# Kernel optimization log

Hardware: AMD Instinct MI355X
Metric: run time of the kernel (lower is better)

The kernel has to match this reference:

```python
import jax, jax.numpy as jnp
import numpy as np

EPS = 1e-5
AVG_D_LOG = 2.302585092994046  # avg_d['log'] = log(10)

N, D, F, FE = 65536, 16, 64, 16
POST_IN = (4 * 3 + 1) * F  # (n_agg*n_scalers + 1) * in_dim = 832


def setup_inputs() -> dict:
    key = jax.random.key(0)
    ks = jax.random.split(key, 8)
    h = jax.random.normal(ks[0], (N, F), dtype=jnp.float32)
    edge_attr = jax.random.normal(ks[1], (N, D, FE), dtype=jnp.float32)
    nbr_idx = jax.random.randint(ks[2], (N, D), 0, N)
    pre_in = 2 * F + FE
    W_pre = jax.random.normal(ks[3], (pre_in, F), dtype=jnp.float32) / np.sqrt(pre_in)
    b_pre = jnp.zeros((F,), dtype=jnp.float32)
    W_post1 = jax.random.normal(ks[4], (POST_IN, F), dtype=jnp.float32) / np.sqrt(POST_IN)
    b_post1 = jnp.zeros((F,), dtype=jnp.float32)
    W_post2 = jax.random.normal(ks[5], (F, F), dtype=jnp.float32) / np.sqrt(F)
    b_post2 = jnp.zeros((F,), dtype=jnp.float32)
    return {"h": h, "edge_attr": edge_attr, "nbr_idx": nbr_idx,
            "W_pre": W_pre, "b_pre": b_pre,
            "W_post1": W_post1, "b_post1": b_post1,
            "W_post2": W_post2, "b_post2": b_post2}


def reference(h, edge_attr, nbr_idx, W_pre, b_pre, W_post1, b_post1, W_post2, b_post2):
    # pretrans: message MLP on cat([src_feat, dst_feat, edge_attr])
    h_src = h[nbr_idx]                                   # [N, D, F]
    h_dst = jnp.broadcast_to(h[:, None, :], h_src.shape)  # [N, D, F]
    z = jnp.concatenate([h_src, h_dst, edge_attr], axis=-1)  # [N, D, 2F+FE]
    e = jax.nn.relu(jnp.einsum('ndi,io->ndo', z, W_pre) + b_pre)  # [N, D, F]

    # multi-aggregator neighbor reduction (dim=-2)
    mean = jnp.mean(e, axis=-2)
    mx = jnp.max(e, axis=-2)
    mn = jnp.min(e, axis=-2)
    var = jax.nn.relu(jnp.mean(e * e, axis=-2) - mean * mean)
    std = jnp.sqrt(var + EPS)
    agg = jnp.concatenate([mean, mx, mn, std], axis=-1)  # [N, 4F]

    # degree scalers (fixed in-degree D)
    logD = jnp.asarray(np.log(D + 1.0), dtype=h.dtype)
    amp = agg * (logD / AVG_D_LOG)
    att = agg * (AVG_D_LOG / logD)
    agg = jnp.concatenate([agg, amp, att], axis=-1)      # [N, 12F]

    # posttrans MLP on cat([h, aggregated]) with residual (in_dim == out_dim)
    x = jnp.concatenate([h, agg], axis=-1)               # [N, 13F]
    x = jax.nn.relu(x @ W_post1 + b_post1)
    x = x @ W_post2 + b_post2
    return x + h
```

## Files before the change

kernel.cpp:

```cpp
#include <hip/hip_runtime.h>
#include <hip/hip_bf16.h>
#include <math.h>
#include <stdint.h>


#define N_NODES 65536
#define NBLK (N_NODES / 16)
#define NITER 4
#define GRID_MAIN (NBLK / NITER)
#define GRID_PREP (NBLK + 64)
#define ASTRIDE 348
#define YSTRIDE 76

typedef float f32x4 __attribute__((ext_vector_type(4)));
typedef float f32x16 __attribute__((ext_vector_type(16)));
typedef short s16x8 __attribute__((ext_vector_type(8)));
typedef unsigned short us4 __attribute__((ext_vector_type(4)));

#define GLL16(SRC, DST)                                                        \
    __builtin_amdgcn_global_load_lds(                                          \
        (const __attribute__((address_space(1))) void*)(SRC),                  \
        (__attribute__((address_space(3))) void*)(DST), 16, 0, 0)

__device__ __forceinline__ unsigned short f2bf(float f) {
    union { float f; unsigned int u; } v; v.f = f;
    unsigned int r = v.u + 0x7fffu + ((v.u >> 16) & 1u);
    return (unsigned short)(r >> 16);
}
__device__ __forceinline__ unsigned short f2bfh(float f) {
    __hip_bfloat16 b = __float2bfloat16(f);
    union { __hip_bfloat16 b; unsigned short u; } v; v.b = b; return v.u;
}
__device__ __forceinline__ float bf2f(unsigned short u) {
    union { unsigned int u; float f; } v; v.u = ((unsigned int)u) << 16; return v.f;
}
__device__ __forceinline__ unsigned char enc_u8(float x) {
    int q = __float2int_rn(x * 16.f) + 128;
    q = q < 0 ? 0 : (q > 255 ? 255 : q);
    return (unsigned char)q;
}

__global__ __launch_bounds__(256) void k_prep(const float* __restrict__ h,
                                              const float* __restrict__ Wpre,
                                              const float* __restrict__ b_pre,
                                              const float* __restrict__ Wp1,
                                              const float* __restrict__ Wp2,
                                              unsigned char* __restrict__ u8,
                                              unsigned short* __restrict__ vbf,
                                              unsigned short* __restrict__ wfullT,
                                              unsigned short* __restrict__ w3T,
                                              unsigned short* __restrict__ wp2T,
                                              float c1, float c2) {
    int t = threadIdx.x;
    if (blockIdx.x >= NBLK) {
        int c = blockIdx.x - NBLK;
        for (int k = t; k < 320; k += 256) {
            float v;
            if (k < 64) v = Wp1[k * 64 + c];
            else {
                int kk = k - 64;
                v = Wp1[(64 + kk) * 64 + c] + c1 * Wp1[(320 + kk) * 64 + c]
                                            + c2 * Wp1[(576 + kk) * 64 + c];
            }
            wfullT[c * 320 + k] = f2bf(v);
        }
        if (t < 16)              w3T[c * 16 + t]         = f2bf(Wpre[(128 + t) * 64 + c]);
        if (t >= 64 && t < 128)  wp2T[c * 64 + (t - 64)] = f2bf(Wp2[(t - 64) * 64 + c]);
        return;
    }

    __shared__ unsigned short hl[16 * 68];
    int lane = t & 63;
    int wv = __builtin_amdgcn_readfirstlane(t) >> 6;
    int c = lane & 15, g = lane >> 4;
    int node0 = blockIdx.x * 16;
    {
        int r = t >> 4, q = t & 15;
        float4 hv = *((const float4*)(h + (size_t)node0 * 64) + t);
        us4 o;
        o.x = f2bfh(hv.x); o.y = f2bfh(hv.y); o.z = f2bfh(hv.z); o.w = f2bfh(hv.w);
        *(us4*)&hl[r * 68 + q * 4] = o;
    }
    s16x8 bf[2][2];
    int woff = (wv < 2) ? 0 : 64;
    #pragma unroll
    for (int i2 = 0; i2 < 2; ++i2) {
        int wcol = ((wv & 1) * 32) + i2 * 16 + c;
        #pragma unroll
        for (int ks = 0; ks < 2; ++ks) {
            #pragma unroll
            for (int j = 0; j < 8; ++j)
                bf[i2][ks][j] = (short)f2bfh(Wpre[(woff + ks * 32 + g * 8 + j) * 64 + wcol]);
        }
    }
    __syncthreads();
    f32x4 acc0 = {0.f, 0.f, 0.f, 0.f}, acc1 = {0.f, 0.f, 0.f, 0.f};
    #pragma unroll
    for (int ks = 0; ks < 2; ++ks) {
        s16x8 a = *(const s16x8*)&hl[c * 68 + ks * 32 + g * 8];
        acc0 = __builtin_amdgcn_mfma_f32_16x16x32_bf16(a, bf[0][ks], acc0, 0, 0, 0);
        acc1 = __builtin_amdgcn_mfma_f32_16x16x32_bf16(a, bf[1][ks], acc1, 0, 0, 0);
    }
    #pragma unroll
    for (int i2 = 0; i2 < 2; ++i2) {
        int dcol = ((wv & 1) * 32) + i2 * 16 + c;
        const f32x4& av = i2 ? acc1 : acc0;
        if (wv < 2) {
            float bp = b_pre[dcol];
            #pragma unroll
            for (int i = 0; i < 4; ++i) {
                int row = g * 4 + i;
                u8[(size_t)(node0 + row) * 64 + dcol] = enc_u8(av[i] + bp);
            }
        } else {
            #pragma unroll
            for (int i = 0; i < 4; ++i) {
                int row = g * 4 + i;
                vbf[(size_t)(node0 + row) * 64 + dcol] = f2bfh(av[i]);
            }
        }
    }
}

__global__ __launch_bounds__(256, 3) void k_main(
    const float* __restrict__ h,
    const float* __restrict__ edge_attr,
    const int* __restrict__ nbr_idx,
    const float* __restrict__ b_post1,
    const float* __restrict__ b_post2,
    const unsigned char* __restrict__ u8,
    const unsigned short* __restrict__ vbf,
    const unsigned short* __restrict__ wfullT,
    const unsigned short* __restrict__ w3T,
    const unsigned short* __restrict__ wp2T,
    float* __restrict__ out) {
    __shared__ unsigned char  u_lds[2][16384];
    __shared__ unsigned short v_lds[2][1024];
    __shared__ unsigned short A_lds[16 * ASTRIDE];
    __shared__ unsigned short y1_lds[16 * YSTRIDE];

    int t = threadIdx.x;
    int lane = t & 63;
    int wv = __builtin_amdgcn_readfirstlane(t) >> 6;
    int c = lane & 15;
    int g = lane >> 4;
    int l32 = lane & 31;
    int h2 = lane >> 5;
    int ct = wv & 1;
    int wr = wv >> 1;
    int colb = ct * 32 + l32;
    int col16 = wv * 16 + c;
    int ch = t & 3;
    int srow = t >> 2;

    s16x8 w3b = *(const s16x8*)&w3T[colb * 16 + h2 * 8];
    float b1c = b_post1[col16];
    float b2c = b_post2[col16];

    int grp0 = blockIdx.x * NITER;
    float4 xaC[4], xbC[4];
    float4 hC;
    int jc[4];

    {
        int j0[4];
        #pragma unroll
        for (int i = 0; i < 4; ++i)
            j0[i] = nbr_idx[(size_t)grp0 * 256 + srow + 64 * i];
        #pragma unroll
        for (int i = 0; i < 4; ++i)
            GLL16(u8 + ((size_t)j0[i] << 6) + ch * 16,
                  &u_lds[0][i * 4096 + wv * 1024]);
        if (wv < 2)
            GLL16((const char*)vbf + ((size_t)grp0 << 11) + (size_t)t * 16,
                  &v_lds[0][wv * 512]);
        const char* eb = (const char*)edge_attr
                       + ((size_t)grp0 * 256 + wr * 32 + l32) * 64 + h2 * 32;
        #pragma unroll
        for (int k = 0; k < 4; ++k) {
            xaC[k] = *(const float4*)(eb + k * 4096);
            xbC[k] = *(const float4*)(eb + k * 4096 + 16);
        }
        hC = *((const float4*)(h + (size_t)grp0 * 1024) + t);
        #pragma unroll
        for (int i = 0; i < 4; ++i)
            jc[i] = nbr_idx[(size_t)(grp0 + 1) * 256 + srow + 64 * i];
        {
            int r = t >> 4, q = t & 15;
            us4 o;
            o.x = f2bfh(hC.x); o.y = f2bfh(hC.y); o.z = f2bfh(hC.z); o.w = f2bfh(hC.w);
            *(us4*)&A_lds[r * ASTRIDE + q * 4] = o;
        }
    }
    __syncthreads();

    #pragma unroll
    for (int it = 0; it < NITER; ++it) {
        const int b = it & 1;
        int grp = grp0 + it;
        size_t node0 = (size_t)grp * 16;
        const bool pf = (it + 1 < NITER);
        int grpn = grp + 1;

        float4 xaN[4], xbN[4];
        float4 hN = {0.f, 0.f, 0.f, 0.f};
        int jn[4] = {0, 0, 0, 0};
        if (pf) {
            #pragma unroll
            for (int i = 0; i < 4; ++i)
                GLL16(u8 + ((size_t)jc[i] << 6) + ch * 16,
                      &u_lds[b ^ 1][i * 4096 + wv * 1024]);
            if (wv < 2)
                GLL16((const char*)vbf + ((size_t)grpn << 11) + (size_t)t * 16,
                      &v_lds[b ^ 1][wv * 512]);
            const char* ebn = (const char*)edge_attr
                            + ((size_t)grpn * 256 + wr * 32 + l32) * 64 + h2 * 32;
            #pragma unroll
            for (int k = 0; k < 4; ++k) {
                xaN[k] = *(const float4*)(ebn + k * 4096);
                xbN[k] = *(const float4*)(ebn + k * 4096 + 16);
            }
            hN = *((const float4*)(h + (size_t)grpn * 1024) + t);
            if (it + 2 < NITER) {
                #pragma unroll
                for (int i = 0; i < 4; ++i)
                    jn[i] = nbr_idx[(size_t)(grp + 2) * 256 + srow + 64 * i];
            }
        }

#define TILEC(IT) {                                                            \
    int rt = wr + 2 * (IT);                                                    \
    s16x8 a;                                                                   \
    a[0] = (short)f2bfh(xaC[IT].x); a[1] = (short)f2bfh(xaC[IT].y);            \
    a[2] = (short)f2bfh(xaC[IT].z); a[3] = (short)f2bfh(xaC[IT].w);            \
    a[4] = (short)f2bfh(xbC[IT].x); a[5] = (short)f2bfh(xbC[IT].y);            \
    a[6] = (short)f2bfh(xbC[IT].z); a[7] = (short)f2bfh(xbC[IT].w);            \
    f32x16 acc = {};                                                           \
    acc = __builtin_amdgcn_mfma_f32_32x32x16_bf16(a, w3b, acc, 0, 0, 0);       \
    const unsigned char* ur = &u_lds[b][(rt * 32 + 4 * h2) * 64 + colb];       \
    float uf[16];                                                              \
    _Pragma("unroll")                                                          \
    for (int q = 0; q < 4; ++q) {                                              \
        uf[4 * q + 0] = (float)ur[(8 * q + 0) * 64];                           \
        uf[4 * q + 1] = (float)ur[(8 * q + 1) * 64];                           \
        uf[4 * q + 2] = (float)ur[(8 * q + 2) * 64];                           \
        uf[4 * q + 3] = (float)ur[(8 * q + 3) * 64];                           \
    }                                                                          \
    float vv0 = bf2f(v_lds[b][(2 * rt + 0) * 64 + colb]) - 8.f;                \
    float vv1 = bf2f(v_lds[b][(2 * rt + 1) * 64 + colb]) - 8.f;                \
    float e0  = fmaxf(fmaf(uf[0],  0.0625f, acc[0]  + vv0), 0.f);              \
    float e1  = fmaxf(fmaf(uf[1],  0.0625f, acc[1]  + vv0), 0.f);              \
    float e2  = fmaxf(fmaf(uf[2],  0.0625f, acc[2]  + vv0), 0.f);              \
    float e3  = fmaxf(fmaf(uf[3],  0.0625f, acc[3]  + vv0), 0.f);              \
    float e4  = fmaxf(fmaf(uf[4],  0.0625f, acc[4]  + vv0), 0.f);              \
    float e5  = fmaxf(fmaf(uf[5],  0.0625f, acc[5]  + vv0), 0.f);              \
    float e6  = fmaxf(fmaf(uf[6],  0.0625f, acc[6]  + vv0), 0.f);              \
    float e7  = fmaxf(fmaf(uf[7],  0.0625f, acc[7]  + vv0), 0.f);              \
    float e8  = fmaxf(fmaf(uf[8],  0.0625f, acc[8]  + vv1), 0.f);              \
    float e9  = fmaxf(fmaf(uf[9],  0.0625f, acc[9]  + vv1), 0.f);              \
    float e10 = fmaxf(fmaf(uf[10], 0.0625f, acc[10] + vv1), 0.f);              \
    float e11 = fmaxf(fmaf(uf[11], 0.0625f, acc[11] + vv1), 0.f);              \
    float e12 = fmaxf(fmaf(uf[12], 0.0625f, acc[12] + vv1), 0.f);              \
    float e13 = fmaxf(fmaf(uf[13], 0.0625f, acc[13] + vv1), 0.f);              \
    float e14 = fmaxf(fmaf(uf[14], 0.0625f, acc[14] + vv1), 0.f);              \
    float e15 = fmaxf(fmaf(uf[15], 0.0625f, acc[15] + vv1), 0.f);              \
    float s1a = ((e0 + e1) + (e2 + e3)) + ((e4 + e5) + (e6 + e7));             \
    float s2a = fmaf(e0, e0, fmaf(e1, e1, fmaf(e2, e2, e3 * e3)))              \
              + fmaf(e4, e4, fmaf(e5, e5, fmaf(e6, e6, e7 * e7)));             \
    float mxa = fmaxf(fmaxf(fmaxf(e0, e1), fmaxf(e2, e3)),                     \
                      fmaxf(fmaxf(e4, e5), fmaxf(e6, e7)));                    \
    float mna = fminf(fminf(fminf(e0, e1), fminf(e2, e3)),                     \
                      fminf(fminf(e4, e5), fminf(e6, e7)));                    \
    float s1b = ((e8 + e9) + (e10 + e11)) + ((e12 + e13) + (e14 + e15));       \
    float s2b = fmaf(e8, e8, fmaf(e9, e9, fmaf(e10, e10, e11 * e11)))          \
              + fmaf(e12, e12, fmaf(e13, e13, fmaf(e14, e14, e15 * e15)));     \
    float mxb = fmaxf(fmaxf(fmaxf(e8, e9), fmaxf(e10, e11)),                   \
                      fmaxf(fmaxf(e12, e13), fmaxf(e14, e15)));                \
    float mnb = fminf(fminf(fminf(e8, e9), fminf(e10, e11)),                   \
                      fminf(fminf(e12, e13), fminf(e14, e15)));                \
    s1a += __shfl_xor(s1a, 32); s2a += __shfl_xor(s2a, 32);                    \
    mxa = fmaxf(mxa, __shfl_xor(mxa, 32)); mna = fminf(mna, __shfl_xor(mna, 32)); \
    s1b += __shfl_xor(s1b, 32); s2b += __shfl_xor(s2b, 32);                    \
    mxb = fmaxf(mxb, __shfl_xor(mxb, 32)); mnb = fminf(mnb, __shfl_xor(mnb, 32)); \
    float S1 = h2 ? s1b : s1a;                                                 \
    float S2 = h2 ? s2b : s2a;                                                 \
    float MX = h2 ? mxb : mxa;                                                 \
    float MN = h2 ? mnb : mna;                                                 \
    float M  = S1 * 0.0625f;                                                   \
    float SD = sqrtf(fmaxf(fmaf(-M, M, S2 * 0.0625f), 0.f) + 1e-5f);           \
    unsigned short* pd = &A_lds[(2 * rt + h2) * ASTRIDE + 64 + colb];          \
    pd[0]   = f2bfh(M);                                                        \
    pd[64]  = f2bfh(MX);                                                       \
    pd[128] = f2bfh(MN);                                                       \
    pd[192] = f2bfh(SD);                                                       \
}
        TILEC(0)
        TILEC(1)
        TILEC(2)
        TILEC(3)
#undef TILEC

        s16x8 wf[10];
        #pragma unroll
        for (int ks = 0; ks < 10; ++ks)
            wf[ks] = *(const s16x8*)&wfullT[col16 * 320 + ks * 32 + g * 8];
        __syncthreads();

        {
            f32x4 y1 = {0.f, 0.f, 0.f, 0.f};
            #pragma unroll
            for (int ks = 0; ks < 10; ++ks) {
                s16x8 a = *(const s16x8*)&A_lds[c * ASTRIDE + ks * 32 + g * 8];
                y1 = __builtin_amdgcn_mfma_f32_16x16x32_bf16(a, wf[ks], y1, 0, 0, 0);
            }
            #pragma unroll
            for (int i = 0; i < 4; ++i)
                y1_lds[(g * 4 + i) * YSTRIDE + col16] = f2bfh(fmaxf(y1[i] + b1c, 0.f));
        }
        s16x8 wp0 = *(const s16x8*)&wp2T[col16 * 64 + 0 * 32 + g * 8];
        s16x8 wp1 = *(const s16x8*)&wp2T[col16 * 64 + 1 * 32 + g * 8];
        __syncthreads();

        if (pf) {
            int r = t >> 4, q = t & 15;
            us4 o;
            o.x = f2bfh(hN.x); o.y = f2bfh(hN.y); o.z = f2bfh(hN.z); o.w = f2bfh(hN.w);
            *(us4*)&A_lds[r * ASTRIDE + q * 4] = o;
        }

        {
            f32x4 o = {0.f, 0.f, 0.f, 0.f};
            s16x8 a0 = *(const s16x8*)&y1_lds[c * YSTRIDE + 0 * 32 + g * 8];
            s16x8 a1 = *(const s16x8*)&y1_lds[c * YSTRIDE + 1 * 32 + g * 8];
            o = __builtin_amdgcn_mfma_f32_16x16x32_bf16(a0, wp0, o, 0, 0, 0);
            o = __builtin_amdgcn_mfma_f32_16x16x32_bf16(a1, wp1, o, 0, 0, 0);
            #pragma unroll
            for (int i = 0; i < 4; ++i) {
                int r = g * 4 + i;
                out[(node0 + r) * 64 + col16] =
                    o[i] + b2c + h[(node0 + r) * 64 + col16];
            }
        }

        if (pf) {
            #pragma unroll
            for (int k = 0; k < 4; ++k) { xaC[k] = xaN[k]; xbC[k] = xbN[k]; }
            hC = hN;
            #pragma unroll
            for (int i = 0; i < 4; ++i) jc[i] = jn[i];
        }
    }
}

extern "C" void kernel_launch(void* const* d_in, const int* in_sizes, int n_in,
                              void* d_out, int out_size, void* d_ws, size_t ws_size,
                              hipStream_t stream) {
    const float* h         = (const float*)d_in[0];
    const float* edge_attr = (const float*)d_in[1];
    const int*   nbr_idx   = (const int*)d_in[2];
    const float* W_pre     = (const float*)d_in[3];
    const float* b_pre     = (const float*)d_in[4];
    const float* W_post1   = (const float*)d_in[5];
    const float* b_post1   = (const float*)d_in[6];
    const float* W_post2   = (const float*)d_in[7];
    const float* b_post2   = (const float*)d_in[8];
    float* out = (float*)d_out;

    size_t need = (size_t)N_NODES * 64
                + (size_t)N_NODES * 64 * 2
                + (64 * 320 + 64 * 16 + 64 * 64) * 2;
    if (ws_size < need) return;
    unsigned char*  u8p    = (unsigned char*)d_ws;
    unsigned short* vbf    = (unsigned short*)(u8p + (size_t)N_NODES * 64);
    unsigned short* wfullT = vbf + (size_t)N_NODES * 64;
    unsigned short* w3T    = wfullT + 64 * 320;
    unsigned short* wp2T   = w3T + 64 * 16;

    double ld = log(16.0 + 1.0);
    const double AVG = 2.302585092994046;
    float c1 = (float)(ld / AVG);
    float c2 = (float)(AVG / ld);

    k_prep<<<GRID_PREP, 256, 0, stream>>>(h, W_pre, b_pre, W_post1, W_post2,
                                          u8p, vbf, wfullT, w3T, wp2T, c1, c2);
    k_main<<<GRID_MAIN, 256, 0, stream>>>(h, edge_attr, nbr_idx, b_post1, b_post2,
                                          u8p, vbf, wfullT, w3T, wp2T, out);
}
```

Baseline: 67.02 us.

## Gather neighbor messages directly from global instead of staging through LDS

Drops the double-buffered global_load_lds staging of gathered u8 neighbor rows and bf16 destination terms. Each lane now loads neighbor indices as vectors and reads its message bytes and destination values straight from global memory inside the tile computation. Freeing that LDS allows raising the launch-bounds occupancy hint from 3 to 4 blocks, and sched barriers plus asm fences keep the next-group prefetch ordered. The trade-off is many small byte-granular global loads that are only partly coalesced, and index-load latency that is no longer hidden by the old pipeline.

```diff
diff --git a/kernel.cpp b/kernel.cpp
--- a/kernel.cpp
+++ b/kernel.cpp
@@ -1,7 +1,6 @@
 #include <hip/hip_runtime.h>
 #include <hip/hip_bf16.h>
 #include <math.h>
-#include <stdint.h>
 
 
 #define N_NODES 65536
@@ -16,11 +15,7 @@
 typedef float f32x16 __attribute__((ext_vector_type(16)));
 typedef short s16x8 __attribute__((ext_vector_type(8)));
 typedef unsigned short us4 __attribute__((ext_vector_type(4)));
-
-#define GLL16(SRC, DST)                                                        \
-    __builtin_amdgcn_global_load_lds(                                          \
-        (const __attribute__((address_space(1))) void*)(SRC),                  \
-        (__attribute__((address_space(3))) void*)(DST), 16, 0, 0)
+typedef int i32x4 __attribute__((ext_vector_type(4)));
 
 __device__ __forceinline__ unsigned short f2bf(float f) {
     union { float f; unsigned int u; } v; v.f = f;
@@ -122,7 +117,7 @@
     }
 }
 
-__global__ __launch_bounds__(256, 3) void k_main(
+__global__ __launch_bounds__(256, 4) void k_main(
     const float* __restrict__ h,
     const float* __restrict__ edge_attr,
     const int* __restrict__ nbr_idx,
@@ -134,8 +129,6 @@
     const unsigned short* __restrict__ w3T,
     const unsigned short* __restrict__ wp2T,
     float* __restrict__ out) {
-    __shared__ unsigned char  u_lds[2][16384];
-    __shared__ unsigned short v_lds[2][1024];
     __shared__ unsigned short A_lds[16 * ASTRIDE];
     __shared__ unsigned short y1_lds[16 * YSTRIDE];
 
@@ -149,31 +142,18 @@
     int ct = wv & 1;
     int wr = wv >> 1;
     int colb = ct * 32 + l32;
+    unsigned cbu = (unsigned)colb;
+    unsigned cb2 = (unsigned)(colb * 2);
     int col16 = wv * 16 + c;
-    int ch = t & 3;
-    int srow = t >> 2;
+    int grp0 = blockIdx.x * NITER;
 
     s16x8 w3b = *(const s16x8*)&w3T[colb * 16 + h2 * 8];
     float b1c = b_post1[col16];
     float b2c = b_post2[col16];
-
-    int grp0 = blockIdx.x * NITER;
+    const unsigned char* ub = u8;
+
     float4 xaC[4], xbC[4];
-    float4 hC;
-    int jc[4];
-
     {
-        int j0[4];
-        #pragma unroll
-        for (int i = 0; i < 4; ++i)
-            j0[i] = nbr_idx[(size_t)grp0 * 256 + srow + 64 * i];
-        #pragma unroll
-        for (int i = 0; i < 4; ++i)
-            GLL16(u8 + ((size_t)j0[i] << 6) + ch * 16,
-                  &u_lds[0][i * 4096 + wv * 1024]);
-        if (wv < 2)
-            GLL16((const char*)vbf + ((size_t)grp0 << 11) + (size_t)t * 16,
-                  &v_lds[0][wv * 512]);
         const char* eb = (const char*)edge_attr
                        + ((size_t)grp0 * 256 + wr * 32 + l32) * 64 + h2 * 32;
         #pragma unroll
@@ -181,89 +161,77 @@
             xaC[k] = *(const float4*)(eb + k * 4096);
             xbC[k] = *(const float4*)(eb + k * 4096 + 16);
         }
-        hC = *((const float4*)(h + (size_t)grp0 * 1024) + t);
-        #pragma unroll
-        for (int i = 0; i < 4; ++i)
-            jc[i] = nbr_idx[(size_t)(grp0 + 1) * 256 + srow + 64 * i];
-        {
-            int r = t >> 4, q = t & 15;
-            us4 o;
-            o.x = f2bfh(hC.x); o.y = f2bfh(hC.y); o.z = f2bfh(hC.z); o.w = f2bfh(hC.w);
-            *(us4*)&A_lds[r * ASTRIDE + q * 4] = o;
-        }
-    }
-    __syncthreads();
+        float4 hv = *((const float4*)(h + (size_t)grp0 * 1024) + t);
+        int r = t >> 4, q = t & 15;
+        us4 o;
+        o.x = f2bfh(hv.x); o.y = f2bfh(hv.y); o.z = f2bfh(hv.z); o.w = f2bfh(hv.w);
+        *(us4*)&A_lds[r * ASTRIDE + q * 4] = o;
+    }
 
     #pragma unroll
     for (int it = 0; it < NITER; ++it) {
-        const int b = it & 1;
         int grp = grp0 + it;
-        size_t node0 = (size_t)grp * 16;
+        int node16 = grp * 16;
+        size_t node0 = (size_t)node16;
         const bool pf = (it + 1 < NITER);
-        int grpn = grp + 1;
 
         float4 xaN[4], xbN[4];
         float4 hN = {0.f, 0.f, 0.f, 0.f};
-        int jn[4] = {0, 0, 0, 0};
         if (pf) {
-            #pragma unroll
-            for (int i = 0; i < 4; ++i)
-                GLL16(u8 + ((size_t)jc[i] << 6) + ch * 16,
-                      &u_lds[b ^ 1][i * 4096 + wv * 1024]);
-            if (wv < 2)
-                GLL16((const char*)vbf + ((size_t)grpn << 11) + (size_t)t * 16,
-                      &v_lds[b ^ 1][wv * 512]);
             const char* ebn = (const char*)edge_attr
-                            + ((size_t)grpn * 256 + wr * 32 + l32) * 64 + h2 * 32;
+                            + ((size_t)(grp + 1) * 256 + wr * 32 + l32) * 64 + h2 * 32;
             #pragma unroll
             for (int k = 0; k < 4; ++k) {
                 xaN[k] = *(const float4*)(ebn + k * 4096);
                 xbN[k] = *(const float4*)(ebn + k * 4096 + 16);
             }
-            hN = *((const float4*)(h + (size_t)grpn * 1024) + t);
-            if (it + 2 < NITER) {
-                #pragma unroll
-                for (int i = 0; i < 4; ++i)
-                    jn[i] = nbr_idx[(size_t)(grp + 2) * 256 + srow + 64 * i];
-            }
-        }
-
-#define TILEC(IT) {                                                            \
+            hN = *((const float4*)(h + (size_t)(grp + 1) * 1024) + t);
+            __builtin_amdgcn_sched_barrier(0);
+        }
+
+        const char* vb = (const char*)vbf + ((unsigned)node16 << 7)
+                       + (unsigned)(wr * 256) + cb2;
+
+#define TILEC(IT, XA, XB) {                                                    \
     int rt = wr + 2 * (IT);                                                    \
+    const int* nbq = nbr_idx + node16 * 16 + rt * 32 + 4 * h2;                 \
+    i32x4 jq0 = *(const i32x4*)(nbq);                                          \
+    i32x4 jq1 = *(const i32x4*)(nbq + 8);                                      \
+    i32x4 jq2 = *(const i32x4*)(nbq + 16);                                     \
+    i32x4 jq3 = *(const i32x4*)(nbq + 24);                                     \
     s16x8 a;                                                                   \
-    a[0] = (short)f2bfh(xaC[IT].x); a[1] = (short)f2bfh(xaC[IT].y);            \
-    a[2] = (short)f2bfh(xaC[IT].z); a[3] = (short)f2bfh(xaC[IT].w);            \
-    a[4] = (short)f2bfh(xbC[IT].x); a[5] = (short)f2bfh(xbC[IT].y);            \
-    a[6] = (short)f2bfh(xbC[IT].z); a[7] = (short)f2bfh(xbC[IT].w);            \
+    a[0] = (short)f2bfh(XA.x); a[1] = (short)f2bfh(XA.y);                      \
+    a[2] = (short)f2bfh(XA.z); a[3] = (short)f2bfh(XA.w);                      \
+    a[4] = (short)f2bfh(XB.x); a[5] = (short)f2bfh(XB.y);                      \
+    a[6] = (short)f2bfh(XB.z); a[7] = (short)f2bfh(XB.w);                      \
     f32x16 acc = {};                                                           \
     acc = __builtin_amdgcn_mfma_f32_32x32x16_bf16(a, w3b, acc, 0, 0, 0);       \
-    const unsigned char* ur = &u_lds[b][(rt * 32 + 4 * h2) * 64 + colb];       \
     float uf[16];                                                              \
     _Pragma("unroll")                                                          \
-    for (int q = 0; q < 4; ++q) {                                              \
-        uf[4 * q + 0] = (float)ur[(8 * q + 0) * 64];                           \
-        uf[4 * q + 1] = (float)ur[(8 * q + 1) * 64];                           \
-        uf[4 * q + 2] = (float)ur[(8 * q + 2) * 64];                           \
-        uf[4 * q + 3] = (float)ur[(8 * q + 3) * 64];                           \
+    for (int i = 0; i < 4; ++i) {                                              \
+        uf[i]      = (float)ub[((unsigned)jq0[i] << 6) + cbu];                 \
+        uf[4 + i]  = (float)ub[((unsigned)jq1[i] << 6) + cbu];                 \
+        uf[8 + i]  = (float)ub[((unsigned)jq2[i] << 6) + cbu];                 \
+        uf[12 + i] = (float)ub[((unsigned)jq3[i] << 6) + cbu];                 \
     }                                                                          \
-    float vv0 = bf2f(v_lds[b][(2 * rt + 0) * 64 + colb]) - 8.f;                \
-    float vv1 = bf2f(v_lds[b][(2 * rt + 1) * 64 + colb]) - 8.f;                \
-    float e0  = fmaxf(fmaf(uf[0],  0.0625f, acc[0]  + vv0), 0.f);              \
-    float e1  = fmaxf(fmaf(uf[1],  0.0625f, acc[1]  + vv0), 0.f);              \
-    float e2  = fmaxf(fmaf(uf[2],  0.0625f, acc[2]  + vv0), 0.f);              \
-    float e3  = fmaxf(fmaf(uf[3],  0.0625f, acc[3]  + vv0), 0.f);              \
-    float e4  = fmaxf(fmaf(uf[4],  0.0625f, acc[4]  + vv0), 0.f);              \
-    float e5  = fmaxf(fmaf(uf[5],  0.0625f, acc[5]  + vv0), 0.f);              \
-    float e6  = fmaxf(fmaf(uf[6],  0.0625f, acc[6]  + vv0), 0.f);              \
-    float e7  = fmaxf(fmaf(uf[7],  0.0625f, acc[7]  + vv0), 0.f);              \
-    float e8  = fmaxf(fmaf(uf[8],  0.0625f, acc[8]  + vv1), 0.f);              \
-    float e9  = fmaxf(fmaf(uf[9],  0.0625f, acc[9]  + vv1), 0.f);              \
-    float e10 = fmaxf(fmaf(uf[10], 0.0625f, acc[10] + vv1), 0.f);              \
-    float e11 = fmaxf(fmaf(uf[11], 0.0625f, acc[11] + vv1), 0.f);              \
-    float e12 = fmaxf(fmaf(uf[12], 0.0625f, acc[12] + vv1), 0.f);              \
-    float e13 = fmaxf(fmaf(uf[13], 0.0625f, acc[13] + vv1), 0.f);              \
-    float e14 = fmaxf(fmaf(uf[14], 0.0625f, acc[14] + vv1), 0.f);              \
-    float e15 = fmaxf(fmaf(uf[15], 0.0625f, acc[15] + vv1), 0.f);              \
+    float vm0 = bf2f(*(const unsigned short*)(vb + (IT) * 512)) - 8.f;         \
+    float vm1 = bf2f(*(const unsigned short*)(vb + (IT) * 512 + 128)) - 8.f;   \
+    float e0  = fmaxf(fmaf(uf[0],  0.0625f, acc[0]  + vm0), 0.f);              \
+    float e1  = fmaxf(fmaf(uf[1],  0.0625f, acc[1]  + vm0), 0.f);              \
+    float e2  = fmaxf(fmaf(uf[2],  0.0625f, acc[2]  + vm0), 0.f);              \
+    float e3  = fmaxf(fmaf(uf[3],  0.0625f, acc[3]  + vm0), 0.f);              \
+    float e4  = fmaxf(fmaf(uf[4],  0.0625f, acc[4]  + vm0), 0.f);              \
+    float e5  = fmaxf(fmaf(uf[5],  0.0625f, acc[5]  + vm0), 0.f);              \
+    float e6  = fmaxf(fmaf(uf[6],  0.0625f, acc[6]  + vm0), 0.f);              \
+    float e7  = fmaxf(fmaf(uf[7],  0.0625f, acc[7]  + vm0), 0.f);              \
+    float e8  = fmaxf(fmaf(uf[8],  0.0625f, acc[8]  + vm1), 0.f);              \
+    float e9  = fmaxf(fmaf(uf[9],  0.0625f, acc[9]  + vm1), 0.f);              \
+    float e10 = fmaxf(fmaf(uf[10], 0.0625f, acc[10] + vm1), 0.f);              \
+    float e11 = fmaxf(fmaf(uf[11], 0.0625f, acc[11] + vm1), 0.f);              \
+    float e12 = fmaxf(fmaf(uf[12], 0.0625f, acc[12] + vm1), 0.f);              \
+    float e13 = fmaxf(fmaf(uf[13], 0.0625f, acc[13] + vm1), 0.f);              \
+    float e14 = fmaxf(fmaf(uf[14], 0.0625f, acc[14] + vm1), 0.f);              \
+    float e15 = fmaxf(fmaf(uf[15], 0.0625f, acc[15] + vm1), 0.f);              \
     float s1a = ((e0 + e1) + (e2 + e3)) + ((e4 + e5) + (e6 + e7));             \
     float s2a = fmaf(e0, e0, fmaf(e1, e1, fmaf(e2, e2, e3 * e3)))              \
               + fmaf(e4, e4, fmaf(e5, e5, fmaf(e6, e6, e7 * e7)));             \
@@ -294,11 +262,20 @@
     pd[128] = f2bfh(MN);                                                       \
     pd[192] = f2bfh(SD);                                                       \
 }
-        TILEC(0)
-        TILEC(1)
-        TILEC(2)
-        TILEC(3)
+        TILEC(0, xaC[0], xbC[0])
+        TILEC(1, xaC[1], xbC[1])
+        TILEC(2, xaC[2], xbC[2])
+        TILEC(3, xaC[3], xbC[3])
 #undef TILEC
+
+        if (pf) {
+            #pragma unroll
+            for (int k = 0; k < 4; ++k) {
+                asm volatile("" :: "v"(xaN[k].x), "v"(xaN[k].y), "v"(xaN[k].z), "v"(xaN[k].w));
+                asm volatile("" :: "v"(xbN[k].x), "v"(xbN[k].y), "v"(xbN[k].z), "v"(xbN[k].w));
+            }
+            asm volatile("" :: "v"(hN.x), "v"(hN.y), "v"(hN.z), "v"(hN.w));
+        }
 
         s16x8 wf[10];
         #pragma unroll
@@ -345,9 +322,6 @@
         if (pf) {
             #pragma unroll
             for (int k = 0; k < 4; ++k) { xaC[k] = xaN[k]; xbC[k] = xbN[k]; }
-            hC = hN;
-            #pragma unroll
-            for (int i = 0; i < 4; ++i) jc[i] = jn[i];
         }
     }
 }
```

Result: slower. 203.7 us (+204.0%).
